# Performance work log

Hardware: AMD Instinct MI355X
Metric: run time of the kernel (lower is better)

## Reference

```python
import jax, jax.numpy as jnp
import numpy as np

N_NODES = 50000
N_EDGES = 600000
IN_CH = 128
HID = 256
OUT_FEAT = 256
OUT_CH = 128
EPS = 1e-12


def _sage_conv(x, src, dst, mask_f, Wl, bl, Wr, n_nodes):
    # PyG SAGEConv: out = lin_l(mean_{j in N(i)} x_j) + lin_r(x_i); L2-normalize rows.
    msg = x[src] * mask_f[:, None]                                  # [E, d] gather
    agg = jax.ops.segment_sum(msg, dst, num_segments=n_nodes)      # [N, d]
    cnt = jax.ops.segment_sum(mask_f, dst, num_segments=n_nodes)   # [N]
    agg = agg / jnp.maximum(cnt, 1.0)[:, None]                      # mean over kept edges
    out = agg @ Wl.T + bl + x @ Wr.T                                 # [N, h]
    nrm = jnp.maximum(jnp.linalg.norm(out, axis=-1, keepdims=True), EPS)
    return out / nrm


def setup_inputs() -> dict:
    key = jax.random.key(0)
    ks = jax.random.split(key, 12)
    x = jax.random.normal(ks[0], (N_NODES, IN_CH), dtype=jnp.float32)
    edge_index = jax.random.randint(ks[1], (2, N_EDGES), 0, N_NODES, dtype=jnp.int32)
    edge_mask = jax.random.bernoulli(ks[2], 0.7, (N_EDGES,))  # dropout_edge p=0.3 keep mask

    def lin(k, fan_out, fan_in):
        s = 1.0 / np.sqrt(fan_in)
        return jax.random.uniform(k, (fan_out, fan_in), jnp.float32, -s, s)

    W1l = lin(ks[3], HID, IN_CH)
    b1 = jnp.zeros((HID,), jnp.float32)
    W1r = lin(ks[4], HID, IN_CH)
    Ws = lin(ks[5], HID, IN_CH)
    bs = jnp.zeros((HID,), jnp.float32)
    W2l = lin(ks[6], OUT_FEAT, HID)
    b2 = jnp.zeros((OUT_FEAT,), jnp.float32)
    W2r = lin(ks[7], OUT_FEAT, HID)
    Wo = lin(ks[8], OUT_CH, OUT_FEAT)
    bo = jnp.zeros((OUT_CH,), jnp.float32)
    return {"x": x, "edge_index": edge_index, "edge_mask": edge_mask,
            "W1l": W1l, "b1": b1, "W1r": W1r, "Ws": Ws, "bs": bs,
            "W2l": W2l, "b2": b2, "W2r": W2r, "Wo": Wo, "bo": bo}


def reference(x, edge_index, edge_mask, W1l, b1, W1r, Ws, bs, W2l, b2, W2r, Wo, bo):
    src, dst = edge_index[0], edge_index[1]
    ones = jnp.ones((src.shape[0],), x.dtype)
    # conv1 uses all edges
    h = _sage_conv(x, src, dst, ones, W1l, b1, W1r, N_NODES)
    h = h + (x @ Ws.T + bs)
    h = jnp.tanh(h)
    # conv2 uses edge-dropped graph (mask = kept edges)
    mask_f = edge_mask.astype(x.dtype)
    h = jnp.tanh(_sage_conv(h, src, dst, mask_f, W2l, b2, W2r, N_NODES))
    return h @ Wo.T + bo
```

## Files before the change

### kernel.cpp

```cpp
#include <hip/hip_runtime.h>
#include <hip/hip_bf16.h>

#define N_NODES 50000
#define N_PAD   50048
#define N_EDGES 600000
#define IN_CH 128
#define HID 256
#define OUT_CH 128

typedef unsigned short u16;
typedef unsigned char u8;
typedef unsigned int u32;

typedef __attribute__((ext_vector_type(8))) short short8;
typedef __attribute__((ext_vector_type(4))) float f32x4;

typedef __attribute__((address_space(3))) u32 as3_u32;
typedef __attribute__((address_space(1))) const u32 as1_u32;

__device__ __forceinline__ float bf2f(u16 v) {
    unsigned u = ((unsigned)v) << 16;
    return __uint_as_float(u);
}
__device__ __forceinline__ u16 f2bf(float f) {
    unsigned u = __float_as_uint(f);
    u += 0x7FFF + ((u >> 16) & 1);
    return (u16)(u >> 16);
}

__device__ __forceinline__ float fast_tanh(float x) {
    float e = __builtin_amdgcn_exp2f(x * 2.88539008177793f);
    return 1.f - 2.f * __builtin_amdgcn_rcpf(e + 1.f);
}

__device__ __forceinline__ void async16(const void* g, void* l) {
    __builtin_amdgcn_global_load_lds((as1_u32*)g, (as3_u32*)l, 16, 0, 0);
}

__device__ __forceinline__ void waitv_sel(int n) {
    if (n >= 10)     { asm volatile("s_waitcnt vmcnt(10)" ::: "memory"); }
    else if (n >= 8) { asm volatile("s_waitcnt vmcnt(8)"  ::: "memory"); }
    else             { asm volatile("s_waitcnt vmcnt(0)"  ::: "memory"); }
    __builtin_amdgcn_sched_barrier(0);
}

__global__ void detect_kernel(const u16* __restrict__ xu, const u8* __restrict__ mb,
                              int* __restrict__ flags) {
    int lane = threadIdx.x & 63;

    int inr = 0;
    {
        u32 w0 = ((const u32*)xu)[lane * 2 + 0];
        u32 w1 = ((const u32*)xu)[lane * 2 + 1];
        u16 h[4] = {(u16)w0, (u16)(w0 >> 16), (u16)w1, (u16)(w1 >> 16)};
#pragma unroll
        for (int j = 0; j < 4; j++) {
            int e = (h[j] >> 7) & 0xFF;
            if (e >= 100 && e <= 133) inr++;
        }
    }

    int c1 = 0, c23 = 0, h3f_1 = 0, h3f_3 = 0;
#pragma unroll
    for (int t = 0; t < 16; t++) {
        u32 w = ((const u32*)mb)[t * 64 + lane];
        u8 b1 = (u8)(w >> 8), b2 = (u8)(w >> 16), b3 = (u8)(w >> 24);
        if (b1) c1++;
        if (b1 == 0x3F) h3f_1 = 1;
        if (b2) c23++;
        if (b3) c23++;
        if (b3 == 0x3F) h3f_3 = 1;
    }

#pragma unroll
    for (int off = 32; off > 0; off >>= 1) {
        inr   += __shfl_xor(inr, off, 64);
        c1    += __shfl_xor(c1, off, 64);
        c23   += __shfl_xor(c23, off, 64);
        h3f_1 |= __shfl_xor(h3f_1, off, 64);
        h3f_3 |= __shfl_xor(h3f_3, off, 64);
    }

    if (lane == 0 && blockIdx.x == 0) {
        flags[0] = (inr >= 200) ? 1 : 0;
        int fmt;
        if (h3f_1) fmt = 3;
        else if (h3f_3) fmt = 2;
        else if (c1 + c23 > 0) fmt = 0;
        else fmt = 1;
        flags[1] = fmt;
    }
}

#define NX (N_NODES * IN_CH)
#define DEGP_N 50176
__global__ void convert_all_kernel(const void* __restrict__ x,
                                   const void* __restrict__ W1l, const void* __restrict__ W1r,
                                   const void* __restrict__ Ws,
                                   const void* __restrict__ W2l, const void* __restrict__ W2r,
                                   const void* __restrict__ Wo,
                                   const void* __restrict__ b1, const void* __restrict__ bs,
                                   const void* __restrict__ b2, const void* __restrict__ bo,
                                   u16* __restrict__ xb, u16* __restrict__ Wc1,
                                   u16* __restrict__ Wsb, u16* __restrict__ Wc2,
                                   u16* __restrict__ Wob, float* __restrict__ biasf,
                                   u32* __restrict__ degp,
                                   const int* __restrict__ flags) {
    int i = blockIdx.x * blockDim.x + threadIdx.x;
    int isbf = flags[0];
    auto cv = [&](const void* s, int idx) -> u16 {
        return isbf ? ((const u16*)s)[idx] : f2bf(((const float*)s)[idx]);
    };
    if (i < NX) { xb[i] = cv(x, i); return; }
    i -= NX;
    if (i < 256 * 256) {
        int n = i >> 8, k = i & 255;
        const void* s = (k < 128) ? W1l : W1r;
        Wc1[i] = cv(s, n * 128 + (k & 127));
        return;
    }
    i -= 256 * 256;
    if (i < 256 * 128) { Wsb[i] = cv(Ws, i); return; }
    i -= 256 * 128;
    if (i < 256 * 512) {
        int n = i >> 9, k = i & 511;
        const void* s = (k < 256) ? W2l : W2r;
        Wc2[i] = cv(s, n * 256 + (k & 255));
        return;
    }
    i -= 256 * 512;
    if (i < 128 * 256) { Wob[i] = cv(Wo, i); return; }
    i -= 128 * 256;
    if (i < 896) {
        const void* s; int idx;
        if (i < 256)      { s = b1; idx = i; }
        else if (i < 512) { s = bs; idx = i - 256; }
        else if (i < 768) { s = b2; idx = i - 512; }
        else              { s = bo; idx = i - 768; }
        biasf[i] = isbf ? bf2f(((const u16*)s)[idx]) : ((const float*)s)[idx];
        return;
    }
    i -= 896;
    if (i < DEGP_N) degp[i] = 0;
}
#define CONV_TOTAL (NX + 256 * 256 + 256 * 128 + 256 * 512 + 128 * 256 + 896 + DEGP_N)

__global__ void hist_kernel(const int* __restrict__ ei, const void* __restrict__ em,
                            u32* __restrict__ degp, u32* __restrict__ rankp,
                            const int* __restrict__ flags) {
    int i = blockIdx.x * blockDim.x + threadIdx.x;
    if (i >= N_EDGES) return;
    int d = ei[N_EDGES + i];
    int fmt = flags[1];
    bool keep;
    if (fmt == 0)      keep = ((const u8*)em)[i] != 0;
    else if (fmt == 1) keep = ((const int*)em)[i] != 0;
    else if (fmt == 2) keep = ((const float*)em)[i] != 0.f;
    else               keep = ((const u16*)em)[i] != 0;
    u32 inc = keep ? 0x10001u : 1u;
    u32 old = atomicAdd(&degp[d], inc);
    rankp[i] = (old & 0xffffu) | (keep ? (old & 0xffff0000u) : 0xffff0000u);
}

__global__ void partial_kernel(const u32* __restrict__ degp, u32* __restrict__ partial) {
    __shared__ u32 sh[256];
    int t = threadIdx.x;
    int i = blockIdx.x * 256 + t;
    sh[t] = (i < N_NODES) ? degp[i] : 0;
    __syncthreads();
    for (int s = 128; s > 0; s >>= 1) {
        if (t < s) sh[t] += sh[t + s];
        __syncthreads();
    }
    if (t == 0) partial[blockIdx.x] = sh[0];
}

__global__ void scanp_kernel(const u32* __restrict__ partial, int* __restrict__ pscan, int nb) {
    __shared__ int sh[256];
    int t = threadIdx.x;
    u32 pv = (t < nb) ? partial[t] : 0;
    int v1 = pv & 0xffff, v2 = pv >> 16;
    sh[t] = v1;
    __syncthreads();
    for (int o = 1; o < 256; o <<= 1) {
        int u = (t >= o) ? sh[t - o] : 0;
        __syncthreads();
        sh[t] += u;
        __syncthreads();
    }
    if (t < nb) pscan[t] = sh[t] - v1;
    __syncthreads();
    sh[t] = v2;
    __syncthreads();
    for (int o = 1; o < 256; o <<= 1) {
        int u = (t >= o) ? sh[t - o] : 0;
        __syncthreads();
        sh[t] += u;
        __syncthreads();
    }
    if (t < nb) pscan[nb + t] = sh[t] - v2;
}

__global__ void rowptr_kernel(const u32* __restrict__ degp, const int* __restrict__ pscan,
                              int* __restrict__ row_ptr, int* __restrict__ row_ptr2, int nb) {
    __shared__ u32 sh[256];
    int t = threadIdx.x;
    int i = blockIdx.x * 256 + t;
    u32 v = (i < N_NODES) ? degp[i] : 0;
    sh[t] = v;
    __syncthreads();
    for (int o = 1; o < 256; o <<= 1) {
        u32 u = (t >= o) ? sh[t - o] : 0;
        __syncthreads();
        sh[t] += u;
        __syncthreads();
    }
    u32 ex = sh[t] - v;
    if (i <= N_NODES) {
        row_ptr[i]  = pscan[blockIdx.x] + (int)(ex & 0xffff);
        row_ptr2[i] = pscan[nb + blockIdx.x] + (int)(ex >> 16);
    }
}

__global__ void scatter_csr_kernel(const int* __restrict__ ei, const u32* __restrict__ rankp,
                                   const int* __restrict__ row_ptr, const int* __restrict__ row_ptr2,
                                   int* __restrict__ srcs, int* __restrict__ srcs2) {
    int i = blockIdx.x * blockDim.x + threadIdx.x;
    if (i >= N_EDGES) return;
    int d = ei[N_EDGES + i];
    int s = ei[i];
    u32 rp = rankp[i];
    srcs[row_ptr[d] + (int)(rp & 0xffffu)] = s;
    u32 kr = rp >> 16;
    if (kr != 0xffffu) srcs2[row_ptr2[d] + (int)kr] = s;
}

__global__ __launch_bounds__(256) void gather1_kernel(const int* __restrict__ row_ptr,
                                                      const int* __restrict__ srcs,
                                                      const u16* __restrict__ xb,
                                                      u16* __restrict__ aggb) {
    int wid = (blockIdx.x * blockDim.x + threadIdx.x) >> 6;
    int lane = threadIdx.x & 63;
    if (wid >= N_NODES) return;
    int start = row_ptr[wid], end = row_ptr[wid + 1];
    int dg = end - start;
    int sv = (lane < dg) ? srcs[start + lane] : 0;
    float a0 = 0.f, a1 = 0.f, b0 = 0.f, b1 = 0.f;
    float c0 = 0.f, c1 = 0.f, d0 = 0.f, d1 = 0.f;
    int n = dg < 64 ? dg : 64;
    int e = 0;
    for (; e + 4 <= n; e += 4) {
        int s0 = __builtin_amdgcn_readlane(sv, e);
        int s1 = __builtin_amdgcn_readlane(sv, e + 1);
        int s2 = __builtin_amdgcn_readlane(sv, e + 2);
        int s3 = __builtin_amdgcn_readlane(sv, e + 3);
        u32 v0 = *(const u32*)(xb + (size_t)s0 * IN_CH + lane * 2);
        u32 v1 = *(const u32*)(xb + (size_t)s1 * IN_CH + lane * 2);
        u32 v2 = *(const u32*)(xb + (size_t)s2 * IN_CH + lane * 2);
        u32 v3 = *(const u32*)(xb + (size_t)s3 * IN_CH + lane * 2);
        a0 += bf2f((u16)v0); a1 += bf2f((u16)(v0 >> 16));
        b0 += bf2f((u16)v1); b1 += bf2f((u16)(v1 >> 16));
        c0 += bf2f((u16)v2); c1 += bf2f((u16)(v2 >> 16));
        d0 += bf2f((u16)v3); d1 += bf2f((u16)(v3 >> 16));
    }
    for (; e < n; e++) {
        int s0 = __builtin_amdgcn_readlane(sv, e);
        u32 v0 = *(const u32*)(xb + (size_t)s0 * IN_CH + lane * 2);
        a0 += bf2f((u16)v0); a1 += bf2f((u16)(v0 >> 16));
    }
    for (e = 64; e < dg; e++) {
        int s0 = srcs[start + e];
        u32 v0 = *(const u32*)(xb + (size_t)s0 * IN_CH + lane * 2);
        a0 += bf2f((u16)v0); a1 += bf2f((u16)(v0 >> 16));
    }
    float inv = 1.f / fmaxf((float)dg, 1.f);
    float rx = (a0 + b0) + (c0 + d0);
    float ry = (a1 + b1) + (c1 + d1);
    u32 o = (u32)f2bf(rx * inv) | ((u32)f2bf(ry * inv) << 16);
    *(u32*)(aggb + (size_t)wid * IN_CH + lane * 2) = o;
}

__global__ __launch_bounds__(256) void gather2_kernel(const int* __restrict__ row_ptr2,
                                                      const int* __restrict__ srcs2,
                                                      const u16* __restrict__ h1b,
                                                      u16* __restrict__ aggb) {
    int wid = (blockIdx.x * blockDim.x + threadIdx.x) >> 6;
    int lane = threadIdx.x & 63;
    if (wid >= N_NODES) return;
    int start = row_ptr2[wid], end = row_ptr2[wid + 1];
    int dg = end - start;
    int sv = (lane < dg) ? srcs2[start + lane] : 0;
    float a0 = 0.f, a1 = 0.f, a2 = 0.f, a3 = 0.f;
    float b0 = 0.f, b1 = 0.f, b2 = 0.f, b3 = 0.f;
    float c0 = 0.f, c1 = 0.f, c2 = 0.f, c3 = 0.f;
    float d0 = 0.f, d1 = 0.f, d2 = 0.f, d3 = 0.f;
    int n = dg < 64 ? dg : 64;
    int e = 0;
    for (; e + 4 <= n; e += 4) {
        int s0 = __builtin_amdgcn_readlane(sv, e);
        int s1 = __builtin_amdgcn_readlane(sv, e + 1);
        int s2 = __builtin_amdgcn_readlane(sv, e + 2);
        int s3 = __builtin_amdgcn_readlane(sv, e + 3);
        uint2 v = *(const uint2*)(h1b + (size_t)s0 * HID + lane * 4);
        uint2 w = *(const uint2*)(h1b + (size_t)s1 * HID + lane * 4);
        uint2 y = *(const uint2*)(h1b + (size_t)s2 * HID + lane * 4);
        uint2 zz = *(const uint2*)(h1b + (size_t)s3 * HID + lane * 4);
        a0 += bf2f((u16)v.x); a1 += bf2f((u16)(v.x >> 16));
        a2 += bf2f((u16)v.y); a3 += bf2f((u16)(v.y >> 16));
        b0 += bf2f((u16)w.x); b1 += bf2f((u16)(w.x >> 16));
        b2 += bf2f((u16)w.y); b3 += bf2f((u16)(w.y >> 16));
        c0 += bf2f((u16)y.x); c1 += bf2f((u16)(y.x >> 16));
        c2 += bf2f((u16)y.y); c3 += bf2f((u16)(y.y >> 16));
        d0 += bf2f((u16)zz.x); d1 += bf2f((u16)(zz.x >> 16));
        d2 += bf2f((u16)zz.y); d3 += bf2f((u16)(zz.y >> 16));
    }
    for (; e < n; e++) {
        int s0 = __builtin_amdgcn_readlane(sv, e);
        uint2 v = *(const uint2*)(h1b + (size_t)s0 * HID + lane * 4);
        a0 += bf2f((u16)v.x); a1 += bf2f((u16)(v.x >> 16));
        a2 += bf2f((u16)v.y); a3 += bf2f((u16)(v.y >> 16));
    }
    for (e = 64; e < dg; e++) {
        int s0 = srcs2[start + e];
        uint2 v = *(const uint2*)(h1b + (size_t)s0 * HID + lane * 4);
        a0 += bf2f((u16)v.x); a1 += bf2f((u16)(v.x >> 16));
        a2 += bf2f((u16)v.y); a3 += bf2f((u16)(v.y >> 16));
    }
    float inv = 1.f / fmaxf((float)dg, 1.f);
    float r0 = (a0 + b0) + (c0 + d0);
    float r1 = (a1 + b1) + (c1 + d1);
    float r2 = (a2 + b2) + (c2 + d2);
    float r3 = (a3 + b3) + (c3 + d3);
    u32 o0 = (u32)f2bf(r0 * inv) | ((u32)f2bf(r1 * inv) << 16);
    u32 o1 = (u32)f2bf(r2 * inv) | ((u32)f2bf(r3 * inv) << 16);
    u16* p = aggb + (size_t)wid * HID + lane * 4;
    *(u32*)p = o0;
    *(u32*)(p + 2) = o1;
}

template<int MODE>
__global__ __launch_bounds__(256, 2) void gemm_staged(
    const u16* __restrict__ A0, const u16* __restrict__ A1,
    const u16* __restrict__ W0, const u16* __restrict__ W1,
    const float* __restrict__ bias0, const float* __restrict__ bias1,
    u16* __restrict__ outb, void* __restrict__ outv, const int* __restrict__ flags) {

    constexpr int NT  = 4;
    constexpr int Nw  = NT * 16;
    constexpr int NKS = (MODE == 1) ? 6 : 8;
    constexpr int ABYTES = 8192;
    constexpr int AARENA = 16384;
    constexpr int BBYTES = 32768;
    __shared__ __align__(16) u8 ldsmem[AARENA + 2 * BBYTES];

    int tid = threadIdx.x;
    int w = tid >> 6, lane = tid & 63;
    int q = lane >> 4, c = lane & 15;
    int m_base = blockIdx.x * 64;
    int rj = lane >> 3, jj = lane & 7;
    int j16 = ((jj ^ rj) << 4);

    f32x4 acc[4][NT], acc2[4][NT];
    const f32x4 z = {0.f, 0.f, 0.f, 0.f};
#pragma unroll
    for (int mt = 0; mt < 4; mt++)
#pragma unroll
        for (int nt = 0; nt < NT; nt++) { acc[mt][nt] = z; acc2[mt][nt] = z; }

    auto stage = [&](int ks, int b) {
        const u16* ap; int astr, kta;
        const u16* wp; int wstr, ktw;
        if (MODE == 1) {
            astr = 128;
            if (ks < 2)      { ap = A0; kta = ks; }
            else if (ks < 4) { ap = A1; kta = ks - 2; }
            else             { ap = A1; kta = ks - 4; }
            if (ks < 4) { wp = W0; wstr = 256; ktw = ks; }
            else        { wp = W1; wstr = 128; ktw = ks - 4; }
        } else {
            astr = 256;
            if (ks < 4) { ap = A0; kta = ks; } else { ap = A1; kta = ks - 4; }
            wp = W0; wstr = 512; ktw = ks;
        }
        if (!(MODE == 1 && ks >= 4)) {
#pragma unroll
            for (int t = 0; t < 2; t++) {
                int r = w * 16 + t * 8;
                const u8* g = (const u8*)(ap + (size_t)(m_base + r + rj) * astr) + kta * 128 + j16;
                async16(g, ldsmem + b * ABYTES + r * 128);
            }
        }
#pragma unroll
        for (int t = 0; t < NT * 2; t++) {
            int n = w * Nw + t * 8;
            const u8* g = (const u8*)(wp + (size_t)(n + rj) * wstr) + ktw * 128 + j16;
            async16(g, ldsmem + AARENA + b * BBYTES + n * 128);
        }
    };

    auto compute = [&](int b, f32x4 (*tgt)[NT]) {
        const u8* ab = ldsmem + b * ABYTES;
        const u8* bb = ldsmem + AARENA + b * BBYTES;
#pragma unroll
        for (int kk = 0; kk < 2; kk++) {
            int sA = (((kk * 4 + q) ^ (c & 7)) << 4);
            short8 af[4], bfr[NT];
#pragma unroll
            for (int mt = 0; mt < 4; mt++)
                af[mt] = *(const short8*)(ab + (mt * 16 + c) * 128 + sA);
#pragma unroll
            for (int nt = 0; nt < NT; nt++)
                bfr[nt] = *(const short8*)(bb + (w * Nw + nt * 16 + c) * 128 + sA);
#pragma unroll
            for (int mt = 0; mt < 4; mt++)
#pragma unroll
                for (int nt = 0; nt < NT; nt++)
                    tgt[mt][nt] = __builtin_amdgcn_mfma_f32_16x16x32_bf16(af[mt], bfr[nt], tgt[mt][nt], 0, 0, 0);
        }
    };

    stage(0, 0);
    stage(1, 1);
    asm volatile("s_waitcnt vmcnt(10)" ::: "memory");
    __builtin_amdgcn_sched_barrier(0);
    __builtin_amdgcn_s_barrier();

#pragma unroll
    for (int ks = 0; ks < NKS; ks++) {
        if (MODE == 1 && ks >= 4) compute(ks & 1, acc2);
        else                      compute(ks & 1, acc);
        if (ks + 1 < NKS) {
            if (ks + 2 < NKS) {
                __builtin_amdgcn_s_barrier();
                stage(ks + 2, ks & 1);
                waitv_sel((MODE == 1 && ks + 2 >= 4) ? 8 : 10);
            } else {
                waitv_sel(0);
            }
            __builtin_amdgcn_s_barrier();
        }
    }
    __syncthreads();

    float* redf = (float*)ldsmem;
    float bcol[NT];
#pragma unroll
    for (int nt = 0; nt < NT; nt++) bcol[nt] = bias0[w * Nw + nt * 16 + c];
    float s[4][4];
#pragma unroll
    for (int mt = 0; mt < 4; mt++)
#pragma unroll
        for (int r = 0; r < 4; r++) {
            float t = 0.f;
#pragma unroll
            for (int nt = 0; nt < NT; nt++) {
                float v = acc[mt][nt][r] + bcol[nt];
                acc[mt][nt][r] = v;
                t += v * v;
            }
            s[mt][r] = t;
        }
#pragma unroll
    for (int off = 1; off < 16; off <<= 1) {
#pragma unroll
        for (int mt = 0; mt < 4; mt++)
#pragma unroll
            for (int r = 0; r < 4; r++)
                s[mt][r] += __shfl_xor(s[mt][r], off, 64);
    }
    if (c == 0) {
#pragma unroll
        for (int mt = 0; mt < 4; mt++)
#pragma unroll
            for (int r = 0; r < 4; r++)
                redf[(mt * 16 + q * 4 + r) * 4 + w] = s[mt][r];
    }
    __syncthreads();
    if (tid < 64) {
        float t = redf[tid * 4] + redf[tid * 4 + 1] + redf[tid * 4 + 2] + redf[tid * 4 + 3];
        redf[256 + tid] = 1.f / fmaxf(sqrtf(t), 1e-12f);
    }
    __syncthreads();

    if (MODE == 1) {
        float b2col[NT];
#pragma unroll
        for (int nt = 0; nt < NT; nt++) b2col[nt] = bias1[w * Nw + nt * 16 + c];
#pragma unroll
        for (int mt = 0; mt < 4; mt++)
#pragma unroll
            for (int r = 0; r < 4; r++) {
                int rl = mt * 16 + q * 4 + r;
                int row = m_base + rl;
                if (row < N_NODES) {
                    float iv = redf[256 + rl];
#pragma unroll
                    for (int nt = 0; nt < NT; nt++) {
                        int col = w * Nw + nt * 16 + c;
                        float t = fast_tanh(acc[mt][nt][r] * iv + acc2[mt][nt][r] + b2col[nt]);
                        float tp = __shfl_xor(t, 1, 64);
                        if (!(lane & 1)) {
                            u32 pk = (u32)f2bf(t) | ((u32)f2bf(tp) << 16);
                            *(u32*)(outb + (size_t)row * HID + col) = pk;
                        }
                    }
                }
            }
    } else {
        u8* h2l = ldsmem + AARENA;
        u8* wol = ldsmem + AARENA + BBYTES;
        int rj2 = lane >> 5, s5 = lane & 31;

        auto stageWo = [&](int half) {
#pragma unroll
            for (int t = 0; t < 8; t++) {
                int rl = w * 16 + t * 2 + rj2;
                const u8* g = (const u8*)W1 + (((size_t)(half * 64 + rl)) << 9)
                            + ((s5 ^ (rl & 7)) << 4);
                async16(g, wol + (w * 16 + t * 2) * 512);
            }
        };

        stageWo(0);
#pragma unroll
        for (int mt = 0; mt < 4; mt++)
#pragma unroll
            for (int r = 0; r < 4; r++) {
                int rl = mt * 16 + q * 4 + r;
                float iv = redf[256 + rl];
#pragma unroll
                for (int nt = 0; nt < NT; nt++) {
                    int k = w * Nw + nt * 16 + c;
                    float t = fast_tanh(acc[mt][nt][r] * iv);
                    float tp = __shfl_xor(t, 1, 64);
                    if (!(lane & 1)) {
                        u32 pk = (u32)f2bf(t) | ((u32)f2bf(tp) << 16);
                        int off = rl * 512 + ((((k >> 3) ^ (rl & 7)) << 4)) + ((k & 7) << 1);
                        *(u32*)(h2l + off) = pk;
                    }
                }
            }
        __syncthreads();

        int isbf = flags[0];
        float bO0 = bias1[w * 16 + c];
        float bO1 = bias1[64 + w * 16 + c];

        auto computeO = [&](f32x4* accO) {
#pragma unroll
            for (int kk = 0; kk < 8; kk++) {
                int sw = (((kk * 4 + q) ^ (c & 7)) << 4);
                short8 bfO = *(const short8*)(wol + (w * 16 + c) * 512 + sw);
#pragma unroll
                for (int mt = 0; mt < 4; mt++) {
                    short8 afO = *(const short8*)(h2l + (mt * 16 + c) * 512 + sw);
                    accO[mt] = __builtin_amdgcn_mfma_f32_16x16x32_bf16(afO, bfO, accO[mt], 0, 0, 0);
                }
            }
        };
        auto storeO = [&](int half, float bO, f32x4* accO) {
#pragma unroll
            for (int mt = 0; mt < 4; mt++)
#pragma unroll
                for (int r = 0; r < 4; r++) {
                    int row = m_base + mt * 16 + q * 4 + r;
                    if (row < N_NODES) {
                        int col = half * 64 + w * 16 + c;
                        float v = accO[mt][r] + bO;
                        if (isbf) {
                            float vp = __shfl_xor(v, 1, 64);
                            if (!(lane & 1))
                                *(u32*)((u16*)outv + (size_t)row * OUT_CH + col) =
                                    (u32)f2bf(v) | ((u32)f2bf(vp) << 16);
                        } else {
                            ((float*)outv)[(size_t)row * OUT_CH + col] = v;
                        }
                    }
                }
        };

        f32x4 accO[4];
#pragma unroll
        for (int mt = 0; mt < 4; mt++) accO[mt] = z;
        computeO(accO);
        __syncthreads();
        stageWo(1);
        storeO(0, bO0, accO);
        __syncthreads();
#pragma unroll
        for (int mt = 0; mt < 4; mt++) accO[mt] = z;
        computeO(accO);
        storeO(1, bO1, accO);
    }
}

extern "C" void kernel_launch(void* const* d_in, const int* in_sizes, int n_in,
                              void* d_out, int out_size, void* d_ws, size_t ws_size,
                              hipStream_t stream) {
    const void* x    = d_in[0];
    const int*  ei   = (const int*)d_in[1];
    const void* em   = d_in[2];
    const void* W1l  = d_in[3];
    const void* b1   = d_in[4];
    const void* W1r  = d_in[5];
    const void* Ws   = d_in[6];
    const void* bs   = d_in[7];
    const void* W2l  = d_in[8];
    const void* b2   = d_in[9];
    const void* W2r  = d_in[10];
    const void* Wo   = d_in[11];
    const void* bo   = d_in[12];

    char* p = (char*)d_ws;
    auto carve = [&](size_t bytes) { char* r = p; p += (bytes + 63) & ~(size_t)63; return r; };
    int*   flags   = (int*)carve(256);
    u16*   xb      = (u16*)carve((size_t)N_PAD * IN_CH * 2);
    u16*   h1b     = (u16*)carve((size_t)N_PAD * HID * 2);
    u16*   aggb    = (u16*)carve((size_t)N_PAD * HID * 2);
    u16*   Wc1     = (u16*)carve(256 * 256 * 2);
    u16*   Wsb     = (u16*)carve(256 * 128 * 2);
    u16*   Wc2     = (u16*)carve(256 * 512 * 2);
    u16*   Wob     = (u16*)carve(128 * 256 * 2);
    float* biasf   = (float*)carve(896 * 4);
    u32*   degp    = (u32*)carve(50176 * 4);
    int*   row_ptr = (int*)carve(50056 * 4);
    int*   row_ptr2= (int*)carve(50056 * 4);
    u32*   partial = (u32*)carve(256 * 4);
    int*   pscan   = (int*)carve(512 * 4);
    u32*   rankp   = (u32*)carve((size_t)N_EDGES * 4);
    int*   srcs    = (int*)carve((size_t)N_EDGES * 4);
    int*   srcs2   = (int*)carve((size_t)N_EDGES * 4);
    float* b1f = biasf, *bsf = biasf + 256, *b2f = biasf + 512, *bof = biasf + 768;
    (void)ws_size; (void)in_sizes; (void)n_in; (void)out_size;

    detect_kernel<<<1, 64, 0, stream>>>((const u16*)x, (const u8*)em, flags);

    convert_all_kernel<<<(CONV_TOTAL + 255) / 256, 256, 0, stream>>>(
        x, W1l, W1r, Ws, W2l, W2r, Wo, b1, bs, b2, bo,
        xb, Wc1, Wsb, Wc2, Wob, biasf, degp, flags);

    hist_kernel<<<(N_EDGES + 255) / 256, 256, 0, stream>>>(ei, em, degp, rankp, flags);
    const int NB = (N_NODES + 255) / 256;
    partial_kernel<<<NB, 256, 0, stream>>>(degp, partial);
    scanp_kernel<<<1, 256, 0, stream>>>(partial, pscan, NB);
    rowptr_kernel<<<NB, 256, 0, stream>>>(degp, pscan, row_ptr, row_ptr2, NB);
    scatter_csr_kernel<<<(N_EDGES + 255) / 256, 256, 0, stream>>>(ei, rankp, row_ptr, row_ptr2, srcs, srcs2);

    const int GB = N_PAD / 64;

    gather1_kernel<<<(N_NODES * 64) / 256, 256, 0, stream>>>(row_ptr, srcs, xb, aggb);
    gemm_staged<1><<<GB, 256, 0, stream>>>(aggb, xb, Wc1, Wsb, b1f, bsf, h1b, nullptr, flags);

    gather2_kernel<<<(N_NODES * 64) / 256, 256, 0, stream>>>(row_ptr2, srcs2, h1b, aggb);
    gemm_staged<2><<<GB, 256, 0, stream>>>(aggb, h1b, Wc2, Wob, b2f, bof, nullptr, d_out, flags);
}
```

Before: 297.7 us.

## Stage GEMM tiles through registers instead of async global-to-LDS loads

Replaces the direct global_load_lds async copies in the dense GEMM kernel with ordinary 16-byte global loads into a register array. The loaded data is written to the alternate LDS buffer after the current tile's MFMA compute. The pipeline becomes issue(k+2) into registers, then commit into LDS after compute, with a single lgkmcnt wait and barrier per step replacing the vmcnt-count-based waits. The goal is to hide global latency behind compute and simplify synchronisation. The cost is about 40 extra VGPRs for the staging array on top of two accumulator sets, which may reduce occupancy or cause spills.

```diff
diff --git a/kernel.cpp b/kernel.cpp
--- a/kernel.cpp
+++ b/kernel.cpp
@@ -35,13 +35,6 @@
 
 __device__ __forceinline__ void async16(const void* g, void* l) {
     __builtin_amdgcn_global_load_lds((as1_u32*)g, (as3_u32*)l, 16, 0, 0);
-}
-
-__device__ __forceinline__ void waitv_sel(int n) {
-    if (n >= 10)     { asm volatile("s_waitcnt vmcnt(10)" ::: "memory"); }
-    else if (n >= 8) { asm volatile("s_waitcnt vmcnt(8)"  ::: "memory"); }
-    else             { asm volatile("s_waitcnt vmcnt(0)"  ::: "memory"); }
-    __builtin_amdgcn_sched_barrier(0);
 }
 
 __global__ void detect_kernel(const u16* __restrict__ xu, const u8* __restrict__ mb,
@@ -367,7 +360,9 @@
 #pragma unroll
         for (int nt = 0; nt < NT; nt++) { acc[mt][nt] = z; acc2[mt][nt] = z; }
 
-    auto stage = [&](int ks, int b) {
+    uint4 L[10];
+
+    auto issue = [&](int ks) {
         const u16* ap; int astr, kta;
         const u16* wp; int wstr, ktw;
         if (MODE == 1) {
@@ -382,19 +377,36 @@
             if (ks < 4) { ap = A0; kta = ks; } else { ap = A1; kta = ks - 4; }
             wp = W0; wstr = 512; ktw = ks;
         }
+        int n = 0;
         if (!(MODE == 1 && ks >= 4)) {
 #pragma unroll
             for (int t = 0; t < 2; t++) {
                 int r = w * 16 + t * 8;
                 const u8* g = (const u8*)(ap + (size_t)(m_base + r + rj) * astr) + kta * 128 + j16;
-                async16(g, ldsmem + b * ABYTES + r * 128);
+                L[n++] = *(const uint4*)g;
             }
         }
 #pragma unroll
         for (int t = 0; t < NT * 2; t++) {
-            int n = w * Nw + t * 8;
-            const u8* g = (const u8*)(wp + (size_t)(n + rj) * wstr) + ktw * 128 + j16;
-            async16(g, ldsmem + AARENA + b * BBYTES + n * 128);
+            int nr = w * Nw + t * 8;
+            const u8* g = (const u8*)(wp + (size_t)(nr + rj) * wstr) + ktw * 128 + j16;
+            L[n++] = *(const uint4*)g;
+        }
+    };
+
+    auto commit = [&](int ks, int b) {
+        int n = 0;
+        if (!(MODE == 1 && ks >= 4)) {
+#pragma unroll
+            for (int t = 0; t < 2; t++) {
+                int r = w * 16 + t * 8;
+                *(uint4*)(ldsmem + b * ABYTES + r * 128 + lane * 16) = L[n++];
+            }
+        }
+#pragma unroll
+        for (int t = 0; t < NT * 2; t++) {
+            int nr = w * Nw + t * 8;
+            *(uint4*)(ldsmem + AARENA + b * BBYTES + nr * 128 + lane * 16) = L[n++];
         }
     };
 
@@ -419,25 +431,25 @@
         }
     };
 
-    stage(0, 0);
-    stage(1, 1);
-    asm volatile("s_waitcnt vmcnt(10)" ::: "memory");
-    __builtin_amdgcn_sched_barrier(0);
-    __builtin_amdgcn_s_barrier();
+    auto lds_barrier = [&]() {
+        asm volatile("s_waitcnt lgkmcnt(0)" ::: "memory");
+        __builtin_amdgcn_sched_barrier(0);
+        __builtin_amdgcn_s_barrier();
+    };
+
+    issue(0);
+    commit(0, 0);
+    issue(1);
+    lds_barrier();
 
 #pragma unroll
     for (int ks = 0; ks < NKS; ks++) {
         if (MODE == 1 && ks >= 4) compute(ks & 1, acc2);
         else                      compute(ks & 1, acc);
         if (ks + 1 < NKS) {
-            if (ks + 2 < NKS) {
-                __builtin_amdgcn_s_barrier();
-                stage(ks + 2, ks & 1);
-                waitv_sel((MODE == 1 && ks + 2 >= 4) ? 8 : 10);
-            } else {
-                waitv_sel(0);
-            }
-            __builtin_amdgcn_s_barrier();
+            commit(ks + 1, (ks + 1) & 1);
+            if (ks + 2 < NKS) issue(ks + 2);
+            lds_barrier();
         }
     }
     __syncthreads();
```

Measured after the change: 402.9 us. 35.3% more time.
